# Optimization experiments

Measured on AMD Instinct MI355X. Metric: run time of the kernel, lower is better.

Reference implementation:

```python
import jax, jax.numpy as jnp
from jax import lax
import numpy as np

B, T, F, H = 4096, 512, 8, 16  # batch, seq, n_features, hidden_dim


def _lstm(x, Wih, Whh, bih, bhh):
    """PyTorch-convention LSTM over batch-first x [B,T,in].
    Returns (h_T [B,H], outputs [B,T,H]). Gate order: i, f, g, o."""
    Bn = x.shape[0]
    Hn = Whh.shape[1]
    xs = jnp.swapaxes(x, 0, 1)                       # [T,B,in]
    x_proj = xs @ Wih.T + (bih + bhh)                # precompute input GEMM: [T,B,4H]

    def step(carry, xp):
        h, c = carry
        gates = xp + h @ Whh.T                       # [B,4H]
        i, f, g, o = jnp.split(gates, 4, axis=-1)
        i = jax.nn.sigmoid(i)
        f = jax.nn.sigmoid(f)
        g = jnp.tanh(g)
        o = jax.nn.sigmoid(o)
        c = f * c + i * g
        h = o * jnp.tanh(c)
        return (h, c), h

    h0 = jnp.zeros((Bn, Hn), x.dtype)
    (hT, _), hs = lax.scan(step, (h0, h0), x_proj)
    return hT, jnp.swapaxes(hs, 0, 1)                # [B,H], [B,T,H]


def setup_inputs() -> dict:
    key = jax.random.key(0)
    ks = jax.random.split(key, 11)
    s_e = 1.0 / np.sqrt(H)
    u = lambda k, shp: jax.random.uniform(k, shp, jnp.float32, -s_e, s_e)
    return {
        "x": jax.random.normal(ks[0], (B, T, F), jnp.float32),
        "enc_Wih": u(ks[1], (4 * H, F)),
        "enc_Whh": u(ks[2], (4 * H, H)),
        "enc_bih": u(ks[3], (4 * H,)),
        "enc_bhh": u(ks[4], (4 * H,)),
        "dec_Wih": u(ks[5], (4 * H, H)),
        "dec_Whh": u(ks[6], (4 * H, H)),
        "dec_bih": u(ks[7], (4 * H,)),
        "dec_bhh": u(ks[8], (4 * H,)),
        "out_W": u(ks[9], (F, H)),
        "out_b": u(ks[10], (F,)),
    }


def reference(x, enc_Wih, enc_Whh, enc_bih, enc_bhh,
              dec_Wih, dec_Whh, dec_bih, dec_bhh, out_W, out_b):
    # encoder: keep only final hidden state h_T
    hT, _ = _lstm(x, enc_Wih, enc_Whh, enc_bih, enc_bhh)   # [B,H]
    # repeat over time: h.squeeze(0).unsqueeze(1).repeat(1,T,1)
    repeated = jnp.broadcast_to(hT[:, None, :], (x.shape[0], x.shape[1], hT.shape[1]))
    _, decoded = _lstm(repeated, dec_Wih, dec_Whh, dec_bih, dec_bhh)  # [B,T,H]
    return decoded @ out_W.T + out_b                       # [B,T,F]
```

## Files before the change

### kernel.cpp

```cpp
#include <hip/hip_runtime.h>

#define B_ 4096
#define T_ 512
#define F_ 8
#define H_ 16

typedef float f32x2 __attribute__((ext_vector_type(2)));
typedef float f32x4v __attribute__((ext_vector_type(4)));

__device__ __forceinline__ f32x2 pkfma(f32x2 a, f32x2 b, f32x2 c) {
    return __builtin_elementwise_fma(a, b, c);
}
#define SV2(v, a, b) __builtin_shufflevector(v, v, a, b)

#define LOG2E 1.442695041f
#define N2LOG2E (-2.885390082f)

__device__ __forceinline__ float sigf(float x) {
    return __builtin_amdgcn_rcpf(1.0f + __builtin_amdgcn_exp2f(-LOG2E * x));
}
__device__ __forceinline__ float tanh_f(float x) {
    return __builtin_fmaf(2.0f,
        __builtin_amdgcn_rcpf(1.0f + __builtin_amdgcn_exp2f(N2LOG2E * x)), -1.0f);
}

template <int K>
__device__ __forceinline__ float rotr(float v) {
    int i = __builtin_bit_cast(int, v);
    return __builtin_bit_cast(float,
        __builtin_amdgcn_update_dpp(i, i, 0x120 + K, 0xF, 0xF, false));
}
__device__ __forceinline__ void rot_all(float ht, float* hr) {
    hr[0]  = ht;
    hr[1]  = rotr<1>(ht);  hr[2]  = rotr<2>(ht);  hr[3]  = rotr<3>(ht);
    hr[4]  = rotr<4>(ht);  hr[5]  = rotr<5>(ht);  hr[6]  = rotr<6>(ht);
    hr[7]  = rotr<7>(ht);  hr[8]  = rotr<8>(ht);  hr[9]  = rotr<9>(ht);
    hr[10] = rotr<10>(ht); hr[11] = rotr<11>(ht); hr[12] = rotr<12>(ht);
    hr[13] = rotr<13>(ht); hr[14] = rotr<14>(ht); hr[15] = rotr<15>(ht);
}

__global__ __launch_bounds__(256, 1) void lstm_ae_kernel(
    const float* __restrict__ x,
    const float* __restrict__ eWih, const float* __restrict__ eWhh,
    const float* __restrict__ ebih, const float* __restrict__ ebhh,
    const float* __restrict__ dWih, const float* __restrict__ dWhh,
    const float* __restrict__ dbih, const float* __restrict__ dbhh,
    const float* __restrict__ oW,   const float* __restrict__ ob,
    float* __restrict__ out)
{
    const int tid = threadIdx.x;
    const int wv  = tid >> 6;
    const int l   = tid & 63;
    const int cw  = l >> 4;
    const int u   = l & 15;
    const int bw  = blockIdx.x * 16 + wv * 4;
    const int b   = bw + cw;

    __shared__ __align__(16) f32x2 xsh[4][4][33][4];

    const f32x2 zero2 = {0.0f, 0.0f};

    float wr[4][16];
    f32x2 wi[4][4];
    float bias[4];
#pragma unroll
    for (int g = 0; g < 4; ++g) {
        const int r = g * 16 + u;
#pragma unroll
        for (int k = 0; k < 16; ++k)
            wr[g][k] = eWhh[r * 16 + ((u - k) & 15)];
        const f32x2* pih = (const f32x2*)(eWih + r * 8);
#pragma unroll
        for (int p = 0; p < 4; ++p) wi[g][p] = pih[p];
        bias[g] = ebih[r] + ebhh[r];
    }

    float c = 0.0f;
    float hrot[16];
#pragma unroll
    for (int k = 0; k < 16; ++k) hrot[k] = 0.0f;

    const int ps = l >> 1, phx = l & 1;
    f32x4v xr[4];
#pragma unroll
    for (int i = 0; i < 4; ++i)
        xr[i] = *(const f32x4v*)(x + ((size_t)(bw + i) * T_ + ps) * F_ + phx * 4);

    for (int c0 = 0; c0 < T_; c0 += 32) {
        __builtin_amdgcn_wave_barrier();
#pragma unroll
        for (int i = 0; i < 4; ++i)
            *(f32x4v*)&xsh[wv][i][ps][phx * 2] = xr[i];
        __builtin_amdgcn_wave_barrier();
        if (c0 + 32 < T_) {
#pragma unroll
            for (int i = 0; i < 4; ++i)
                xr[i] = *(const f32x4v*)(
                    x + ((size_t)(bw + i) * T_ + (c0 + 32 + ps)) * F_ + phx * 4);
        }
        for (int s = 0; s < 32; ++s) {
            f32x4v xq0 = *(const f32x4v*)&xsh[wv][cw][s][0];
            f32x4v xq1 = *(const f32x4v*)&xsh[wv][cw][s][2];
            f32x2 x0 = SV2(xq0, 0, 1), x1 = SV2(xq0, 2, 3);
            f32x2 x2 = SV2(xq1, 0, 1), x3 = SV2(xq1, 2, 3);

            float sg[4];
#pragma unroll
            for (int g = 0; g < 4; ++g) {
                f32x2 pa = pkfma(wi[g][0], x0, f32x2{bias[g], 0.0f});
                f32x2 pb = pkfma(wi[g][1], x1, zero2);
                pa = pkfma(wi[g][2], x2, pa);
                pb = pkfma(wi[g][3], x3, pb);
                f32x2 ts = pa + pb;
                float cA = ts.x + ts.y, cB = 0.0f;
#pragma unroll
                for (int k = 0; k < 16; k += 2) {
                    cA = __builtin_fmaf(wr[g][k],     hrot[k],     cA);
                    cB = __builtin_fmaf(wr[g][k + 1], hrot[k + 1], cB);
                }
                sg[g] = cA + cB;
            }
            const float gi = sigf(sg[0]);
            const float gf = sigf(sg[1]);
            const float gg = tanh_f(sg[2]);
            const float go = sigf(sg[3]);
            c = __builtin_fmaf(gf, c, gi * gg);
            const float ht = go * tanh_f(c);
            rot_all(ht, hrot);
        }
    }

    float wd[4][16], wo[16], xp[4];
#pragma unroll
    for (int g = 0; g < 4; ++g) {
        const int r = g * 16 + u;
        float a = 0.0f;
#pragma unroll
        for (int k = 0; k < 16; ++k) {
            wd[g][k] = dWhh[r * 16 + ((u - k) & 15)];
            a = __builtin_fmaf(dWih[r * 16 + ((u - k) & 15)], hrot[k], a);
        }
        xp[g] = dbih[r] + dbhh[r] + a;
    }
#pragma unroll
    for (int k = 0; k < 16; ++k)
        wo[k] = oW[(u & 7) * 16 + ((u - k) & 15)];
    const float obv = ob[u & 7];
    const bool st = (u < 8);
    float* outp = out + (size_t)b * (T_ * F_);

    c = 0.0f;
#pragma unroll
    for (int k = 0; k < 16; ++k) hrot[k] = 0.0f;

    for (int t = 0; t < T_; ++t) {
        float sg[4];
#pragma unroll
        for (int g = 0; g < 4; ++g) {
            float cA = xp[g], cB = 0.0f;
#pragma unroll
            for (int k = 0; k < 16; k += 2) {
                cA = __builtin_fmaf(wd[g][k],     hrot[k],     cA);
                cB = __builtin_fmaf(wd[g][k + 1], hrot[k + 1], cB);
            }
            sg[g] = cA + cB;
        }
        const float gi = sigf(sg[0]);
        const float gf = sigf(sg[1]);
        const float gg = tanh_f(sg[2]);
        const float go = sigf(sg[3]);
        c = __builtin_fmaf(gf, c, gi * gg);
        const float ht = go * tanh_f(c);
        rot_all(ht, hrot);

        float oA = obv, oB = 0.0f;
#pragma unroll
        for (int k = 0; k < 16; k += 2) {
            oA = __builtin_fmaf(wo[k],     hrot[k],     oA);
            oB = __builtin_fmaf(wo[k + 1], hrot[k + 1], oB);
        }
        if (st) outp[t * F_ + u] = oA + oB;
    }
}

extern "C" void kernel_launch(void* const* d_in, const int* in_sizes, int n_in,
                              void* d_out, int out_size, void* d_ws, size_t ws_size,
                              hipStream_t stream) {
    (void)in_sizes; (void)n_in; (void)d_ws; (void)ws_size; (void)out_size;
    lstm_ae_kernel<<<dim3(B_ / 16), dim3(256), 0, stream>>>(
        (const float*)d_in[0],
        (const float*)d_in[1], (const float*)d_in[2],
        (const float*)d_in[3], (const float*)d_in[4],
        (const float*)d_in[5], (const float*)d_in[6],
        (const float*)d_in[7], (const float*)d_in[8],
        (const float*)d_in[9], (const float*)d_in[10],
        (float*)d_out);
}
```

Before: 406.6 us.

## Split LSTM hidden-dim reduction across two half-waves to double parallelism

Each wave now handles 2 batch rows instead of 4. The upper and lower 32 lanes each compute half of the 16-term recurrent dot product (8 terms) and combine the halves with a cross-half shuffle. This roughly halves the serial FMA chain per timestep, doubles the block count and relaxes launch bounds so two blocks can share a CU. It also prefetches the next x vector from shared memory one step ahead and unrolls the decoder loop by 2. In exchange it adds a cross-lane shuffle per gate on the critical path, duplicates the activation math in both halves, and uses twice as many threads for the same batch.

```diff
diff --git a/kernel.cpp b/kernel.cpp
--- a/kernel.cpp
+++ b/kernel.cpp
@@ -5,13 +5,7 @@
 #define F_ 8
 #define H_ 16
 
-typedef float f32x2 __attribute__((ext_vector_type(2)));
 typedef float f32x4v __attribute__((ext_vector_type(4)));
-
-__device__ __forceinline__ f32x2 pkfma(f32x2 a, f32x2 b, f32x2 c) {
-    return __builtin_elementwise_fma(a, b, c);
-}
-#define SV2(v, a, b) __builtin_shufflevector(v, v, a, b)
 
 #define LOG2E 1.442695041f
 #define N2LOG2E (-2.885390082f)
@@ -30,16 +24,13 @@
     return __builtin_bit_cast(float,
         __builtin_amdgcn_update_dpp(i, i, 0x120 + K, 0xF, 0xF, false));
 }
-__device__ __forceinline__ void rot_all(float ht, float* hr) {
-    hr[0]  = ht;
-    hr[1]  = rotr<1>(ht);  hr[2]  = rotr<2>(ht);  hr[3]  = rotr<3>(ht);
-    hr[4]  = rotr<4>(ht);  hr[5]  = rotr<5>(ht);  hr[6]  = rotr<6>(ht);
-    hr[7]  = rotr<7>(ht);  hr[8]  = rotr<8>(ht);  hr[9]  = rotr<9>(ht);
-    hr[10] = rotr<10>(ht); hr[11] = rotr<11>(ht); hr[12] = rotr<12>(ht);
-    hr[13] = rotr<13>(ht); hr[14] = rotr<14>(ht); hr[15] = rotr<15>(ht);
+__device__ __forceinline__ float ror8_hi(float v) {
+    int i = __builtin_bit_cast(int, v);
+    return __builtin_bit_cast(float,
+        __builtin_amdgcn_update_dpp(i, i, 0x128, 0xC, 0xF, false));
 }
 
-__global__ __launch_bounds__(256, 1) void lstm_ae_kernel(
+__global__ __launch_bounds__(256, 2) void lstm_ae_kernel(
     const float* __restrict__ x,
     const float* __restrict__ eWih, const float* __restrict__ eWhh,
     const float* __restrict__ ebih, const float* __restrict__ ebhh,
@@ -51,135 +42,144 @@
     const int tid = threadIdx.x;
     const int wv  = tid >> 6;
     const int l   = tid & 63;
-    const int cw  = l >> 4;
+    const int ch  = (l >> 4) & 1;
+    const int kh  = l >> 5;
     const int u   = l & 15;
-    const int bw  = blockIdx.x * 16 + wv * 4;
-    const int b   = bw + cw;
+    const int b0  = blockIdx.x * 8 + wv * 2;
+    const int b   = b0 + ch;
 
-    __shared__ __align__(16) f32x2 xsh[4][4][33][4];
+    __shared__ __align__(16) float xsh[4][2][33][8];
 
-    const f32x2 zero2 = {0.0f, 0.0f};
-
-    float wr[4][16];
-    f32x2 wi[4][4];
-    float bias[4];
+    float wr[4][8], wi4[4][4], bias0[4];
 #pragma unroll
     for (int g = 0; g < 4; ++g) {
         const int r = g * 16 + u;
 #pragma unroll
-        for (int k = 0; k < 16; ++k)
-            wr[g][k] = eWhh[r * 16 + ((u - k) & 15)];
-        const f32x2* pih = (const f32x2*)(eWih + r * 8);
+        for (int j = 0; j < 8; ++j)
+            wr[g][j] = eWhh[r * 16 + ((u - j - 8 * kh) & 15)];
 #pragma unroll
-        for (int p = 0; p < 4; ++p) wi[g][p] = pih[p];
-        bias[g] = ebih[r] + ebhh[r];
+        for (int j = 0; j < 4; ++j)
+            wi4[g][j] = eWih[r * 8 + kh * 4 + j];
+        bias0[g] = (kh == 0) ? (ebih[r] + ebhh[r]) : 0.0f;
     }
 
     float c = 0.0f;
-    float hrot[16];
+    float hj[8];
 #pragma unroll
-    for (int k = 0; k < 16; ++k) hrot[k] = 0.0f;
+    for (int j = 0; j < 8; ++j) hj[j] = 0.0f;
 
-    const int ps = l >> 1, phx = l & 1;
-    f32x4v xr[4];
-#pragma unroll
-    for (int i = 0; i < 4; ++i)
-        xr[i] = *(const f32x4v*)(x + ((size_t)(bw + i) * T_ + ps) * F_ + phx * 4);
+    const int sA = l >> 1, hA = (l & 1) * 4;
+    const float* xb0 = x + (size_t)b0 * (T_ * F_);
+    const float* xb1 = x + (size_t)(b0 + 1) * (T_ * F_);
+    f32x4v xr0 = *(const f32x4v*)(xb0 + sA * F_ + hA);
+    f32x4v xr1 = *(const f32x4v*)(xb1 + sA * F_ + hA);
 
     for (int c0 = 0; c0 < T_; c0 += 32) {
         __builtin_amdgcn_wave_barrier();
-#pragma unroll
-        for (int i = 0; i < 4; ++i)
-            *(f32x4v*)&xsh[wv][i][ps][phx * 2] = xr[i];
+        *(f32x4v*)&xsh[wv][0][sA][hA] = xr0;
+        *(f32x4v*)&xsh[wv][1][sA][hA] = xr1;
         __builtin_amdgcn_wave_barrier();
         if (c0 + 32 < T_) {
-#pragma unroll
-            for (int i = 0; i < 4; ++i)
-                xr[i] = *(const f32x4v*)(
-                    x + ((size_t)(bw + i) * T_ + (c0 + 32 + ps)) * F_ + phx * 4);
+            xr0 = *(const f32x4v*)(xb0 + (c0 + 32 + sA) * F_ + hA);
+            xr1 = *(const f32x4v*)(xb1 + (c0 + 32 + sA) * F_ + hA);
         }
+        f32x4v xv = *(const f32x4v*)&xsh[wv][ch][0][kh * 4];
         for (int s = 0; s < 32; ++s) {
-            f32x4v xq0 = *(const f32x4v*)&xsh[wv][cw][s][0];
-            f32x4v xq1 = *(const f32x4v*)&xsh[wv][cw][s][2];
-            f32x2 x0 = SV2(xq0, 0, 1), x1 = SV2(xq0, 2, 3);
-            f32x2 x2 = SV2(xq1, 0, 1), x3 = SV2(xq1, 2, 3);
-
+            f32x4v nx = *(const f32x4v*)&xsh[wv][ch][s + 1][kh * 4];
             float sg[4];
 #pragma unroll
             for (int g = 0; g < 4; ++g) {
-                f32x2 pa = pkfma(wi[g][0], x0, f32x2{bias[g], 0.0f});
-                f32x2 pb = pkfma(wi[g][1], x1, zero2);
-                pa = pkfma(wi[g][2], x2, pa);
-                pb = pkfma(wi[g][3], x3, pb);
-                f32x2 ts = pa + pb;
-                float cA = ts.x + ts.y, cB = 0.0f;
+                float a = bias0[g];
+                a = __builtin_fmaf(wi4[g][0], xv[0], a);
+                a = __builtin_fmaf(wi4[g][1], xv[1], a);
+                a = __builtin_fmaf(wi4[g][2], xv[2], a);
+                a = __builtin_fmaf(wi4[g][3], xv[3], a);
 #pragma unroll
-                for (int k = 0; k < 16; k += 2) {
-                    cA = __builtin_fmaf(wr[g][k],     hrot[k],     cA);
-                    cB = __builtin_fmaf(wr[g][k + 1], hrot[k + 1], cB);
-                }
-                sg[g] = cA + cB;
+                for (int j = 0; j < 8; ++j)
+                    a = __builtin_fmaf(wr[g][j], hj[j], a);
+                sg[g] = a;
             }
+            sg[0] += __shfl_xor(sg[0], 32, 64);
+            sg[1] += __shfl_xor(sg[1], 32, 64);
+            sg[2] += __shfl_xor(sg[2], 32, 64);
+            sg[3] += __shfl_xor(sg[3], 32, 64);
+
             const float gi = sigf(sg[0]);
             const float gf = sigf(sg[1]);
             const float gg = tanh_f(sg[2]);
             const float go = sigf(sg[3]);
             c = __builtin_fmaf(gf, c, gi * gg);
             const float ht = go * tanh_f(c);
-            rot_all(ht, hrot);
+
+            const float h8 = ror8_hi(ht);
+            hj[0] = h8;
+            hj[1] = rotr<1>(h8); hj[2] = rotr<2>(h8); hj[3] = rotr<3>(h8);
+            hj[4] = rotr<4>(h8); hj[5] = rotr<5>(h8); hj[6] = rotr<6>(h8);
+            hj[7] = rotr<7>(h8);
+            xv = nx;
         }
     }
 
-    float wd[4][16], wo[16], xp[4];
+    float wd[4][8], wo[8], xpp[4];
 #pragma unroll
     for (int g = 0; g < 4; ++g) {
         const int r = g * 16 + u;
-        float a = 0.0f;
+        float a = (kh == 0) ? (dbih[r] + dbhh[r]) : 0.0f;
 #pragma unroll
-        for (int k = 0; k < 16; ++k) {
-            wd[g][k] = dWhh[r * 16 + ((u - k) & 15)];
-            a = __builtin_fmaf(dWih[r * 16 + ((u - k) & 15)], hrot[k], a);
+        for (int j = 0; j < 8; ++j) {
+            const int idx = (u - j - 8 * kh) & 15;
+            a = __builtin_fmaf(dWih[r * 16 + idx], hj[j], a);
+            wd[g][j] = dWhh[r * 16 + idx];
         }
-        xp[g] = dbih[r] + dbhh[r] + a;
+        xpp[g] = a;
     }
+    const int fo = u & 7;
 #pragma unroll
-    for (int k = 0; k < 16; ++k)
-        wo[k] = oW[(u & 7) * 16 + ((u - k) & 15)];
-    const float obv = ob[u & 7];
-    const bool st = (u < 8);
+    for (int j = 0; j < 8; ++j)
+        wo[j] = oW[fo * 16 + ((u - j - 8 * kh) & 15)];
+    const float obv = ob[fo];
+    const bool st = (u < 8) && (kh == 0);
     float* outp = out + (size_t)b * (T_ * F_);
 
     c = 0.0f;
 #pragma unroll
-    for (int k = 0; k < 16; ++k) hrot[k] = 0.0f;
+    for (int j = 0; j < 8; ++j) hj[j] = 0.0f;
 
+#pragma unroll 2
     for (int t = 0; t < T_; ++t) {
         float sg[4];
 #pragma unroll
         for (int g = 0; g < 4; ++g) {
-            float cA = xp[g], cB = 0.0f;
+            float a = xpp[g];
 #pragma unroll
-            for (int k = 0; k < 16; k += 2) {
-                cA = __builtin_fmaf(wd[g][k],     hrot[k],     cA);
-                cB = __builtin_fmaf(wd[g][k + 1], hrot[k + 1], cB);
-            }
-            sg[g] = cA + cB;
+            for (int j = 0; j < 8; ++j)
+                a = __builtin_fmaf(wd[g][j], hj[j], a);
+            sg[g] = a;
         }
+        sg[0] += __shfl_xor(sg[0], 32, 64);
+        sg[1] += __shfl_xor(sg[1], 32, 64);
+        sg[2] += __shfl_xor(sg[2], 32, 64);
+        sg[3] += __shfl_xor(sg[3], 32, 64);
+
         const float gi = sigf(sg[0]);
         const float gf = sigf(sg[1]);
         const float gg = tanh_f(sg[2]);
         const float go = sigf(sg[3]);
         c = __builtin_fmaf(gf, c, gi * gg);
         const float ht = go * tanh_f(c);
-        rot_all(ht, hrot);
 
-        float oA = obv, oB = 0.0f;
+        const float h8 = ror8_hi(ht);
+        hj[0] = h8;
+        hj[1] = rotr<1>(h8); hj[2] = rotr<2>(h8); hj[3] = rotr<3>(h8);
+        hj[4] = rotr<4>(h8); hj[5] = rotr<5>(h8); hj[6] = rotr<6>(h8);
+        hj[7] = rotr<7>(h8);
+
+        float oa = 0.0f;
 #pragma unroll
-        for (int k = 0; k < 16; k += 2) {
-            oA = __builtin_fmaf(wo[k],     hrot[k],     oA);
-            oB = __builtin_fmaf(wo[k + 1], hrot[k + 1], oB);
-        }
-        if (st) outp[t * F_ + u] = oA + oB;
+        for (int j = 0; j < 8; ++j)
+            oa = __builtin_fmaf(wo[j], hj[j], oa);
+        oa += __shfl_xor(oa, 32, 64);
+        if (st) outp[t * F_ + u] = oa + obv;
     }
 }
 
@@ -187,7 +187,7 @@
                               void* d_out, int out_size, void* d_ws, size_t ws_size,
                               hipStream_t stream) {
     (void)in_sizes; (void)n_in; (void)d_ws; (void)ws_size; (void)out_size;
-    lstm_ae_kernel<<<dim3(B_ / 16), dim3(256), 0, stream>>>(
+    lstm_ae_kernel<<<dim3(B_ / 8), dim3(256), 0, stream>>>(
         (const float*)d_in[0],
         (const float*)d_in[1], (const float*)d_in[2],
         (const float*)d_in[3], (const float*)d_in[4],
```

After: 487.9 us. 20.0% more time.
